# Performance work log

Measured on AMD Instinct MI355X. Metric: run time of the kernel, lower is better.

## Reference

```python
import jax, jax.numpy as jnp
import numpy as np

NX, NTEST, DX, DY = 8192, 8192, 32, 32
VAR_EPS = 0.01   # params['var_eps']
L_MEAN = 8.0     # fit kernel lengthscale after l_scale adjustment
L_VAR = 8.0


def _rbf(X, Y, l):
    # pairwise squared distances: [Nx, Nq]
    d2 = (jnp.sum(X * X, axis=1)[:, None]
          + jnp.sum(Y * Y, axis=1)[None, :]
          - 2.0 * (X @ Y.T))
    return jnp.exp(-jnp.maximum(d2, 0.0) / (2.0 * l * l))


def setup_inputs() -> dict:
    key = jax.random.key(0)
    ks = jax.random.split(key, 10)
    inp = {
        'x_mu':   jax.random.normal(ks[0], (NTEST, DX), jnp.float32),
        'y_eta':  jax.random.normal(ks[1], (NTEST, DY), jnp.float32),
        'y_mean': jax.random.normal(ks[2], (NTEST, DY), jnp.float32),
        'y_var':  jax.random.normal(ks[3], (NTEST, DY), jnp.float32) * 0.1,
        'X_mean': jax.random.normal(ks[4], (NX, DX + DY), jnp.float32),
        'X_var':  jax.random.normal(ks[5], (NX, DX + 2 * DY), jnp.float32),
        'Z_mean': jax.random.normal(ks[6], (NX, DY), jnp.float32),
        'Z_var':  jax.random.normal(ks[7], (NX, DY), jnp.float32),
        # precomputed inverse Gram matrices (stand-ins with same compute pattern)
        'kXXmean_inv': jax.random.normal(ks[8], (NX, NX), jnp.float32) * 0.001,
        'kXXvar_inv':  jax.random.normal(ks[9], (NX, NX), jnp.float32) * 0.001,
    }
    return inp


def reference(x_mu, y_eta, y_mean, y_var, X_mean, X_var, Z_mean, Z_var,
              kXXmean_inv, kXXvar_inv):
    # map_mean: x_mean = [x_mu, y_mean + y_var]
    x_mean = jnp.concatenate([x_mu, y_mean + y_var], axis=1)          # [Nq, DX+DY]
    Lambda_mean = kXXmean_inv @ Z_mean                                # [Nx, DY]
    z_mean = _rbf(X_mean, x_mean, L_MEAN).T @ Lambda_mean             # [Nq, DY]

    # map_var: x_var = [x_mu, var_eps * flip(y_eta), y_mean + y_var]
    x_var = jnp.concatenate(
        [x_mu, VAR_EPS * jnp.flip(y_eta, axis=0), y_mean + y_var], axis=1)
    Lambda_var = kXXvar_inv @ Z_var                                   # [Nx, DY]
    z_var = _rbf(X_var, x_var, L_VAR).T @ Lambda_var                  # [Nq, DY]

    # transported sample: (y_mean + z_mean) + (y_var + z_var)
    return (y_mean + z_mean) + (y_var + z_var)
```

## Files before the change

kernel.cpp:

```cpp
#include <hip/hip_runtime.h>
#include <stdint.h>

#define NXR 8192
#define NQR 8192
#define DMEAN 64
#define DVAR 96
#define DYC 32

typedef float f32x4 __attribute__((ext_vector_type(4)));
typedef __bf16 bf16x8 __attribute__((ext_vector_type(8)));
typedef unsigned short us4v __attribute__((ext_vector_type(4)));

__device__ __forceinline__ unsigned short f2bf(float f) {
    union { float f; uint32_t u; } v; v.f = f;
    uint32_t r = (v.u + 0x7FFFu + ((v.u >> 16) & 1u)) >> 16;
    return (unsigned short)r;
}
__device__ __forceinline__ float bf2f(unsigned short b) {
    union { uint32_t u; float f; } v; v.u = ((uint32_t)b) << 16;
    return v.f;
}
__device__ __forceinline__ int perm_idx(int k, int c) {
    return (k >> 5) * 1024 + (c >> 4) * 512 +
           ((((k >> 3) & 3) * 16 + (c & 15)) * 8) + (k & 7);
}

__global__ __launch_bounds__(256) void k_prep(
    const float* __restrict__ x_mu, const float* __restrict__ y_eta,
    const float* __restrict__ y_mean, const float* __restrict__ y_var,
    const float* __restrict__ X_mean, const float* __restrict__ X_var,
    const float* __restrict__ Z_mean, const float* __restrict__ Z_var,
    unsigned short* __restrict__ Qm, unsigned short* __restrict__ Qv,
    unsigned short* __restrict__ Xm, unsigned short* __restrict__ Xv,
    unsigned short* __restrict__ Zpm, unsigned short* __restrict__ Zpv,
    float* __restrict__ qn_m, float* __restrict__ qn_v,
    float* __restrict__ Xn_m, float* __restrict__ Xn_v,
    float* __restrict__ out)
{
    int w = threadIdx.x >> 6;
    int lane = threadIdx.x & 63;
    int row = blockIdx.x * 4 + w;

    float accq_m = 0.f, accq_v = 0.f;
    if (lane < 32) {
        int c = lane;
        float xm = x_mu[row * 32 + c];
        float s  = y_mean[row * 32 + c] + y_var[row * 32 + c];
        float e  = 0.01f * y_eta[(NQR - 1 - row) * 32 + c];
        unsigned short bx = f2bf(xm), bs = f2bf(s), be = f2bf(e);
        Qm[row * DMEAN + c] = bx;  Qm[row * DMEAN + 32 + c] = bs;
        Qv[row * DVAR + c] = bx;   Qv[row * DVAR + 32 + c] = be;
        Qv[row * DVAR + 64 + c] = bs;
        out[row * 32 + c] = s;
        Zpm[perm_idx(row, c)] = f2bf(Z_mean[row * 32 + c]);
        Zpv[perm_idx(row, c)] = f2bf(Z_var[row * 32 + c]);
        float fx = bf2f(bx), fs = bf2f(bs), fe = bf2f(be);
        accq_m = fx * fx + fs * fs;
        accq_v = fx * fx + fe * fe + fs * fs;
    }
    float a = X_mean[row * DMEAN + lane];
    unsigned short ba = f2bf(a);
    Xm[row * DMEAN + lane] = ba;
    float fa = bf2f(ba);
    float accx_m = fa * fa;

    float b0 = X_var[row * DVAR + lane];
    unsigned short bb0 = f2bf(b0);
    Xv[row * DVAR + lane] = bb0;
    float fb0 = bf2f(bb0);
    float accx_v = fb0 * fb0;
    if (lane < 32) {
        float b1 = X_var[row * DVAR + 64 + lane];
        unsigned short bb1 = f2bf(b1);
        Xv[row * DVAR + 64 + lane] = bb1;
        float fb1 = bf2f(bb1);
        accx_v += fb1 * fb1;
    }
    for (int o = 32; o >= 1; o >>= 1) {
        accq_m += __shfl_xor(accq_m, o, 64);
        accq_v += __shfl_xor(accq_v, o, 64);
        accx_m += __shfl_xor(accx_m, o, 64);
        accx_v += __shfl_xor(accx_v, o, 64);
    }
    if (lane == 0) {
        qn_m[row] = accq_m; qn_v[row] = accq_v;
        Xn_m[row] = accx_m; Xn_v[row] = accx_v;
    }
}

__global__ __launch_bounds__(256, 4) void k_lambda(
    const float* __restrict__ kXXm, const float* __restrict__ kXXv,
    const unsigned short* __restrict__ Zpm, const unsigned short* __restrict__ Zpv,
    unsigned short* __restrict__ Lpm, unsigned short* __restrict__ Lpv)
{
    __shared__ float red[4][64][8];
    int b = blockIdx.x;
    int mat = b & 1;
    int rg = b >> 1;
    const float* A = mat ? kXXv : kXXm;
    const unsigned short* Zp = mat ? Zpv : Zpm;
    unsigned short* Lp = mat ? Lpv : Lpm;

    int w = threadIdx.x >> 6, lane = threadIdx.x & 63;
    int r0 = rg * 16;
    int arow = r0 + (lane & 15);
    int kgrp = (lane >> 4) * 8;
    const float* Arow = A + (size_t)arow * NXR;

    f32x4 acc0 = {0.f, 0.f, 0.f, 0.f}, acc1 = {0.f, 0.f, 0.f, 0.f};
    f32x4 bA[4][2], bB[4][2];
    int kb = w * 64;

#define LOAD_BODY(BUF, KB0) do { \
    _Pragma("unroll") \
    for (int j = 0; j < 4; ++j) { \
        const f32x4* p = (const f32x4*)(Arow + (((KB0) + j) << 5) + kgrp); \
        BUF[j][0] = p[0]; BUF[j][1] = p[1]; \
    } } while (0)

#define PROC_BODY(BUF, KB0) do { \
    _Pragma("unroll") \
    for (int j = 0; j < 4; ++j) { \
        union { unsigned short u[8]; bf16x8 v; } af; \
        _Pragma("unroll") \
        for (int q2 = 0; q2 < 4; ++q2) { \
            af.u[q2] = f2bf(BUF[j][0][q2]); af.u[4 + q2] = f2bf(BUF[j][1][q2]); \
        } \
        const unsigned short* zb = Zp + (((size_t)((KB0) + j)) << 10) + lane * 8; \
        bf16x8 bz0 = *(const bf16x8*)(zb); \
        bf16x8 bz1 = *(const bf16x8*)(zb + 512); \
        acc0 = __builtin_amdgcn_mfma_f32_16x16x32_bf16(af.v, bz0, acc0, 0, 0, 0); \
        acc1 = __builtin_amdgcn_mfma_f32_16x16x32_bf16(af.v, bz1, acc1, 0, 0, 0); \
    } } while (0)

    LOAD_BODY(bA, kb);
#pragma unroll 1
    for (int s = 0; s < 7; ++s) {
        LOAD_BODY(bB, kb + 4);
        PROC_BODY(bA, kb);
        LOAD_BODY(bA, kb + 8);
        PROC_BODY(bB, kb + 4);
        kb += 8;
    }
    LOAD_BODY(bB, kb + 4);
    PROC_BODY(bA, kb);
    PROC_BODY(bB, kb + 4);
#undef LOAD_BODY
#undef PROC_BODY

    *(f32x4*)&red[w][lane][0] = acc0;
    *(f32x4*)&red[w][lane][4] = acc1;
    __syncthreads();
    int t = threadIdx.x;
    int row = t >> 4, c16 = t & 15;
    int ls = (row >> 2) * 16 + c16;
    int rr = row & 3;
    float v0 = red[0][ls][rr] + red[1][ls][rr] + red[2][ls][rr] + red[3][ls][rr];
    float v1 = red[0][ls][4 + rr] + red[1][ls][4 + rr] +
               red[2][ls][4 + rr] + red[3][ls][4 + rr];
    Lp[perm_idx(r0 + row, c16)]      = f2bf(v0);
    Lp[perm_idx(r0 + row, c16 + 16)] = f2bf(v1);
}

__global__ __launch_bounds__(256) void k_transport(
    const unsigned short* __restrict__ Qm, const unsigned short* __restrict__ Qv,
    const unsigned short* __restrict__ Xm, const unsigned short* __restrict__ Xv,
    const float* __restrict__ qn_m, const float* __restrict__ qn_v,
    const float* __restrict__ Xn_m, const float* __restrict__ Xn_v,
    const unsigned short* __restrict__ Lpm, const unsigned short* __restrict__ Lpv,
    float* __restrict__ out)
{
    __shared__ unsigned short KT[4][16 * 40];
    int b = blockIdx.x;
    int mat = b & 1;
    int split = (b >> 1) & 3;
    int qb = b >> 3;
    const unsigned short* Q = mat ? Qv : Qm;
    const unsigned short* X = mat ? Xv : Xm;
    const float* qn = mat ? qn_v : qn_m;
    const float* Xn = mat ? Xn_v : Xn_m;
    const unsigned short* Lp = mat ? Lpv : Lpm;
    const int D = mat ? DVAR : DMEAN;
    const int nk0 = mat ? 3 : 2;

    int w = threadIdx.x >> 6, lane = threadIdx.x & 63;
    int q0 = qb * 64 + w * 16;
    int qrow = q0 + (lane & 15);
    int g = lane >> 4;

    bf16x8 Qf[3];
    for (int c0 = 0; c0 < nk0; ++c0)
        Qf[c0] = *(const bf16x8*)(Q + (size_t)qrow * D + c0 * 32 + g * 8);
    float qn_c = qn[qrow];
    unsigned short* lds = KT[w];

    f32x4 z0 = {0.f, 0.f, 0.f, 0.f}, z1 = {0.f, 0.f, 0.f, 0.f};
    for (int xb = 0; xb < 64; ++xb) {
        int x0 = split * 2048 + xb * 32;
#pragma unroll
        for (int sub = 0; sub < 2; ++sub) {
            int xrow = x0 + sub * 16 + (lane & 15);
            const unsigned short* Xr = X + (size_t)xrow * D + g * 8;
            f32x4 s = {0.f, 0.f, 0.f, 0.f};
            s = __builtin_amdgcn_mfma_f32_16x16x32_bf16(*(const bf16x8*)(Xr), Qf[0], s, 0, 0, 0);
            s = __builtin_amdgcn_mfma_f32_16x16x32_bf16(*(const bf16x8*)(Xr + 32), Qf[1], s, 0, 0, 0);
            if (nk0 == 3)
                s = __builtin_amdgcn_mfma_f32_16x16x32_bf16(*(const bf16x8*)(Xr + 64), Qf[2], s, 0, 0, 0);
            int xnb = x0 + sub * 16 + g * 4;
            f32x4 xn4 = *(const f32x4*)(Xn + xnb);
            us4v kv;
#pragma unroll
            for (int r = 0; r < 4; ++r) {
                float d2 = xn4[r] + qn_c - 2.0f * s[r];
                d2 = fmaxf(d2, 0.0f);
                kv[r] = f2bf(__expf(-d2 * 0.0078125f));
            }
            *(us4v*)(lds + (lane & 15) * 40 + sub * 16 + g * 4) = kv;
        }
        asm volatile("s_waitcnt lgkmcnt(0)" ::: "memory");
        bf16x8 Kf = *(const bf16x8*)(lds + (lane & 15) * 40 + g * 8);
        const unsigned short* lpb = Lp + (size_t)(x0 >> 5) * 1024 + lane * 8;
        bf16x8 l0 = *(const bf16x8*)(lpb);
        bf16x8 l1 = *(const bf16x8*)(lpb + 512);
        z0 = __builtin_amdgcn_mfma_f32_16x16x32_bf16(Kf, l0, z0, 0, 0, 0);
        z1 = __builtin_amdgcn_mfma_f32_16x16x32_bf16(Kf, l1, z1, 0, 0, 0);
    }
    int rbase = q0 + g * 4;
    int c0 = lane & 15;
#pragma unroll
    for (int r = 0; r < 4; ++r) {
        atomicAdd(&out[(rbase + r) * 32 + c0], z0[r]);
        atomicAdd(&out[(rbase + r) * 32 + c0 + 16], z1[r]);
    }
}

extern "C" void kernel_launch(void* const* d_in, const int* in_sizes, int n_in,
                              void* d_out, int out_size, void* d_ws, size_t ws_size,
                              hipStream_t stream) {
    const float* x_mu   = (const float*)d_in[0];
    const float* y_eta  = (const float*)d_in[1];
    const float* y_mean = (const float*)d_in[2];
    const float* y_var  = (const float*)d_in[3];
    const float* X_mean = (const float*)d_in[4];
    const float* X_var  = (const float*)d_in[5];
    const float* Z_mean = (const float*)d_in[6];
    const float* Z_var  = (const float*)d_in[7];
    const float* kXXm   = (const float*)d_in[8];
    const float* kXXv   = (const float*)d_in[9];
    float* out = (float*)d_out;

    char* ws = (char*)d_ws;
    size_t off = 0;
    auto carve = [&](size_t bytes) { char* p = ws + off; off += (bytes + 255) & ~(size_t)255; return p; };
    unsigned short* Qm  = (unsigned short*)carve(NQR * DMEAN * 2);
    unsigned short* Qv  = (unsigned short*)carve(NQR * DVAR * 2);
    unsigned short* Xm  = (unsigned short*)carve(NXR * DMEAN * 2);
    unsigned short* Xv  = (unsigned short*)carve(NXR * DVAR * 2);
    unsigned short* Zpm = (unsigned short*)carve(NXR * DYC * 2);
    unsigned short* Zpv = (unsigned short*)carve(NXR * DYC * 2);
    unsigned short* Lpm = (unsigned short*)carve(NXR * DYC * 2);
    unsigned short* Lpv = (unsigned short*)carve(NXR * DYC * 2);
    float* qn_m = (float*)carve(NQR * 4);
    float* qn_v = (float*)carve(NQR * 4);
    float* Xn_m = (float*)carve(NXR * 4);
    float* Xn_v = (float*)carve(NXR * 4);

    k_prep<<<dim3(2048), dim3(256), 0, stream>>>(
        x_mu, y_eta, y_mean, y_var, X_mean, X_var, Z_mean, Z_var,
        Qm, Qv, Xm, Xv, Zpm, Zpv, qn_m, qn_v, Xn_m, Xn_v, out);
    k_lambda<<<dim3(1024), dim3(256), 0, stream>>>(kXXm, kXXv, Zpm, Zpv, Lpm, Lpv);
    k_transport<<<dim3(1024), dim3(256), 0, stream>>>(
        Qm, Qv, Xm, Xv, qn_m, qn_v, Xn_m, Xn_v, Lpm, Lpv, out);
}
```

Before: 716.0 us.

## Stream Lambda GEMM operands through LDS via async global_load_lds

Replaces the register-prefetched fp32 loads of the inverse Gram matrix and Z in k_lambda with direct global-to-LDS transfers. Each warp double-buffers these in its own LDS slice, uses an XOR-swizzled layout, and synchronises with explicit vmcnt waits. The aim is to cut register pressure and raise memory-level parallelism on this bandwidth-bound matrix-vector-like product. The cost is fewer bytes in flight per wave, 32KB of LDS per block that may limit occupancy, and reliance on hand-placed waitcnt ordering.

```diff
diff --git a/kernel.cpp b/kernel.cpp
--- a/kernel.cpp
+++ b/kernel.cpp
@@ -23,6 +23,12 @@
 __device__ __forceinline__ int perm_idx(int k, int c) {
     return (k >> 5) * 1024 + (c >> 4) * 512 +
            ((((k >> 3) & 3) * 16 + (c & 15)) * 8) + (k & 7);
+}
+
+typedef const __attribute__((address_space(1))) uint32_t* as1_u32p;
+typedef __attribute__((address_space(3))) uint32_t* as3_u32p;
+__device__ __forceinline__ void gl_lds16(const void* g, void* l) {
+    __builtin_amdgcn_global_load_lds((as1_u32p)g, (as3_u32p)l, 16, 0, 0);
 }
 
 __global__ __launch_bounds__(256) void k_prep(
@@ -93,7 +99,7 @@
     const unsigned short* __restrict__ Zpm, const unsigned short* __restrict__ Zpv,
     unsigned short* __restrict__ Lpm, unsigned short* __restrict__ Lpv)
 {
-    __shared__ float red[4][64][8];
+    __shared__ __align__(16) char smem[32768];
     int b = blockIdx.x;
     int mat = b & 1;
     int rg = b >> 1;
@@ -103,56 +109,59 @@
 
     int w = threadIdx.x >> 6, lane = threadIdx.x & 63;
     int r0 = rg * 16;
-    int arow = r0 + (lane & 15);
-    int kgrp = (lane >> 4) * 8;
-    const float* Arow = A + (size_t)arow * NXR;
+    char* wb = smem + w * 8192;
+
+    int rtA  = lane >> 3;
+    int srcA = ((lane & 7) * 16) ^ (rtA << 4);
+    const char* A0 = (const char*)A + ((size_t)(r0 + rtA) * NXR) * 4
+                     + (size_t)w * 8192 + srcA;
+    const char* A1 = A0 + (size_t)8 * NXR * 4;
+    const char* Zb = (const char*)Zp + (size_t)w * 64 * 2048 + lane * 16;
+
+    int rt = lane & 15, g = lane >> 4;
+    int ro0 = rt * 128 + (((g * 32) + 0)  ^ ((rt & 7) << 4));
+    int ro1 = rt * 128 + (((g * 32) + 16) ^ ((rt & 7) << 4));
 
     f32x4 acc0 = {0.f, 0.f, 0.f, 0.f}, acc1 = {0.f, 0.f, 0.f, 0.f};
-    f32x4 bA[4][2], bB[4][2];
-    int kb = w * 64;
-
-#define LOAD_BODY(BUF, KB0) do { \
-    _Pragma("unroll") \
-    for (int j = 0; j < 4; ++j) { \
-        const f32x4* p = (const f32x4*)(Arow + (((KB0) + j) << 5) + kgrp); \
-        BUF[j][0] = p[0]; BUF[j][1] = p[1]; \
-    } } while (0)
-
-#define PROC_BODY(BUF, KB0) do { \
-    _Pragma("unroll") \
-    for (int j = 0; j < 4; ++j) { \
-        union { unsigned short u[8]; bf16x8 v; } af; \
-        _Pragma("unroll") \
-        for (int q2 = 0; q2 < 4; ++q2) { \
-            af.u[q2] = f2bf(BUF[j][0][q2]); af.u[4 + q2] = f2bf(BUF[j][1][q2]); \
-        } \
-        const unsigned short* zb = Zp + (((size_t)((KB0) + j)) << 10) + lane * 8; \
-        bf16x8 bz0 = *(const bf16x8*)(zb); \
-        bf16x8 bz1 = *(const bf16x8*)(zb + 512); \
-        acc0 = __builtin_amdgcn_mfma_f32_16x16x32_bf16(af.v, bz0, acc0, 0, 0, 0); \
-        acc1 = __builtin_amdgcn_mfma_f32_16x16x32_bf16(af.v, bz1, acc1, 0, 0, 0); \
-    } } while (0)
-
-    LOAD_BODY(bA, kb);
+
+    auto stage = [&](int t) {
+        char* base = wb + (t & 1) * 4096;
+        size_t ko = (size_t)t * 128;
+        gl_lds16(A0 + ko, base);
+        gl_lds16(A1 + ko, base + 1024);
+        gl_lds16(Zb + (size_t)t * 2048, base + 2048);
+        gl_lds16(Zb + (size_t)t * 2048 + 1024, base + 3072);
+    };
+    auto process = [&](int t) {
+        char* base = wb + (t & 1) * 4096;
+        f32x4 a0 = *(const f32x4*)(base + ro0);
+        f32x4 a1 = *(const f32x4*)(base + ro1);
+        bf16x8 bz0 = *(const bf16x8*)(base + 2048 + lane * 16);
+        bf16x8 bz1 = *(const bf16x8*)(base + 3072 + lane * 16);
+        union { unsigned short u[8]; bf16x8 v; } af;
+#pragma unroll
+        for (int j = 0; j < 4; ++j) { af.u[j] = f2bf(a0[j]); af.u[4 + j] = f2bf(a1[j]); }
+        acc0 = __builtin_amdgcn_mfma_f32_16x16x32_bf16(af.v, bz0, acc0, 0, 0, 0);
+        acc1 = __builtin_amdgcn_mfma_f32_16x16x32_bf16(af.v, bz1, acc1, 0, 0, 0);
+    };
+
+    stage(0);
 #pragma unroll 1
-    for (int s = 0; s < 7; ++s) {
-        LOAD_BODY(bB, kb + 4);
-        PROC_BODY(bA, kb);
-        LOAD_BODY(bA, kb + 8);
-        PROC_BODY(bB, kb + 4);
-        kb += 8;
-    }
-    LOAD_BODY(bB, kb + 4);
-    PROC_BODY(bA, kb);
-    PROC_BODY(bB, kb + 4);
-#undef LOAD_BODY
-#undef PROC_BODY
-
+    for (int t = 0; t < 63; ++t) {
+        stage(t + 1);
+        asm volatile("s_waitcnt vmcnt(4)" ::: "memory");
+        process(t);
+    }
+    asm volatile("s_waitcnt vmcnt(0)" ::: "memory");
+    process(63);
+
+    __syncthreads();
+    float (*red)[64][8] = (float (*)[64][8])smem;
     *(f32x4*)&red[w][lane][0] = acc0;
     *(f32x4*)&red[w][lane][4] = acc1;
     __syncthreads();
-    int t = threadIdx.x;
-    int row = t >> 4, c16 = t & 15;
+    int tix = threadIdx.x;
+    int row = tix >> 4, c16 = tix & 15;
     int ls = (row >> 2) * 16 + c16;
     int rr = row & 3;
     float v0 = red[0][ls][rr] + red[1][ls][rr] + red[2][ls][rr] + red[3][ls][rr];
```

After: 711.7 us. No clear change (-0.6%).
